# Performance work log

Measured on AMD Instinct MI355X. Metric: run time of the kernel, lower is better.

Reference implementation:

```python
import jax, jax.numpy as jnp
import numpy as np

N_NODES = 100000
N_EDGES = 1600000
IN_DIM = 256
OUT_DIM = 128
BATCH = 8192
SLOPE = 0.1
EPS = 1e-8


def setup_inputs() -> dict:
    key = jax.random.key(0)
    k1, k2, k3, k4, k5, k6, k7 = jax.random.split(key, 7)
    feats = jax.random.normal(k1, (N_NODES, IN_DIM), dtype=jnp.float32)
    W = jax.random.normal(k2, (IN_DIM, OUT_DIM), dtype=jnp.float32) / np.sqrt(IN_DIM)
    b = jax.random.normal(k3, (OUT_DIM,), dtype=jnp.float32) * 0.01
    a = jax.random.normal(k4, (2 * OUT_DIM,), dtype=jnp.float32) / np.sqrt(2 * OUT_DIM)
    r = jax.random.randint(k5, (N_EDGES,), 0, N_NODES, dtype=jnp.int64)
    c = jax.random.randint(k6, (N_EDGES,), 0, N_NODES, dtype=jnp.int64)
    batch_idx = jax.random.randint(k7, (BATCH,), 0, N_NODES, dtype=jnp.int64)
    return {"feats": feats, "W": W, "b": b, "a": a, "r": r, "c": c, "batch_idx": batch_idx}


def reference(feats, W, b, a, r, c, batch_idx):
    d = W.shape[1]
    new_emb = feats @ W + b                      # [N, d]
    # [h_r || h_c] @ a  ==  h_r @ a[:d] + h_c @ a[d:]
    s_src = new_emb @ a[:d]                      # [N]
    s_dst = new_emb @ a[d:]                      # [N]
    e = jnp.exp(jax.nn.leaky_relu(s_src[r] + s_dst[c], negative_slope=SLOPE))  # [E]
    denom = jax.ops.segment_sum(e, r, num_segments=N_NODES)                    # [N]
    num = jax.ops.segment_sum(e[:, None] * new_emb[c], r, num_segments=N_NODES)  # [N, d]
    out = num / (denom[:, None] + EPS)
    return out[batch_idx]
```

## Files before the change

kernel.cpp:

```cpp
#include <hip/hip_runtime.h>

#define N_NODES 100000
#define N_EDGES 1600000
#define IN_DIM  256
#define OUT_DIM 128
#define BATCH_N 8192
#define SLOPE   0.1f
#define EPS_V   1e-8f
#define BUCKET_CAP 96

__global__ __launch_bounds__(256) void setup_kernel(const float* __restrict__ W,
                                                    const float* __restrict__ b,
                                                    const float* __restrict__ a,
                                                    const int* __restrict__ batch_idx,
                                                    int* __restrict__ slot,
                                                    int* __restrict__ cursor,
                                                    float* __restrict__ uv,
                                                    float* __restrict__ consts) {
  const int blk = blockIdx.x, t = threadIdx.x;
  if (blk < 32) {
    int i = blk * 256 + t;
    slot[batch_idx[i]] = i;
    cursor[i] = 0;
    return;
  }
  float su = 0.f, sv = 0.f;
  for (int j = 0; j < OUT_DIM; j++) {
    float w = W[t * OUT_DIM + j];
    su += w * a[j];
    sv += w * a[OUT_DIM + j];
  }
  uv[t] = su;
  uv[IN_DIM + t] = sv;

  __shared__ float red[256];
  float pb = (t < OUT_DIM) ? b[t] : 0.f;
  red[t] = (t < OUT_DIM) ? pb * a[t] : 0.f;
  __syncthreads();
  for (int off = 128; off > 0; off >>= 1) {
    if (t < off) red[t] += red[t + off];
    __syncthreads();
  }
  if (t == 0) consts[0] = red[0];
  __syncthreads();
  red[t] = (t < OUT_DIM) ? pb * a[OUT_DIM + t] : 0.f;
  __syncthreads();
  for (int off = 128; off > 0; off >>= 1) {
    if (t < off) red[t] += red[t + off];
    __syncthreads();
  }
  if (t == 0) consts[1] = red[0];
}

__global__ __launch_bounds__(256) void scores_kernel(const float* __restrict__ feats,
                                                     const float* __restrict__ uv,
                                                     const float* __restrict__ consts,
                                                     float* __restrict__ s_src,
                                                     float* __restrict__ s_dst) {
  int wid = (blockIdx.x * blockDim.x + threadIdx.x) >> 6;
  int lane = threadIdx.x & 63;
  if (wid >= N_NODES) return;
  float4 f  = *(const float4*)&feats[(size_t)wid * IN_DIM + lane * 4];
  float4 u4 = *(const float4*)&uv[lane * 4];
  float4 v4 = *(const float4*)&uv[IN_DIM + lane * 4];
  float p1 = f.x * u4.x + f.y * u4.y + f.z * u4.z + f.w * u4.w;
  float p2 = f.x * v4.x + f.y * v4.y + f.z * v4.z + f.w * v4.w;
#pragma unroll
  for (int s = 32; s > 0; s >>= 1) {
    p1 += __shfl_xor(p1, s);
    p2 += __shfl_xor(p2, s);
  }
  if (lane == 0) {
    s_src[wid] = p1 + consts[0];
    s_dst[wid] = p2 + consts[1];
  }
}

__global__ __launch_bounds__(256) void scatter_kernel(const int* __restrict__ r, const int* __restrict__ c,
                                                      const int* __restrict__ slot,
                                                      const int* __restrict__ batch_idx,
                                                      const float* __restrict__ s_src,
                                                      const float* __restrict__ s_dst,
                                                      int* __restrict__ cursor,
                                                      int* __restrict__ bucket_c, float* __restrict__ bucket_e) {
  int i = blockIdx.x * blockDim.x + threadIdx.x;
  if (i >= N_EDGES) return;
  int rr = r[i];
  int sl = slot[rr];
  if (sl < 0 || sl >= BATCH_N) return;
  if (batch_idx[sl] != rr) return;
  int cc = c[i];
  float x = s_src[rr] + s_dst[cc];
  float lr = x > 0.f ? x : SLOPE * x;
  float e = expf(lr);
  int pos = atomicAdd(&cursor[sl], 1);
  if (pos < BUCKET_CAP) {
    bucket_c[sl * BUCKET_CAP + pos] = cc;
    bucket_e[sl * BUCKET_CAP + pos] = e;
  }
}

__global__ __launch_bounds__(256) void agg_kernel(const float* __restrict__ feats,
                                                  const int* __restrict__ cursor,
                                                  const int* __restrict__ bucket_c,
                                                  const float* __restrict__ bucket_e,
                                                  float* __restrict__ aggw,
                                                  float* __restrict__ scale_b) {
  __shared__ int   sc[BUCKET_CAP];
  __shared__ float se[BUCKET_CAP];
  __shared__ float red[4][256];
  __shared__ float dred[4];
  const int sl = blockIdx.x;
  const int t = threadIdx.x, w = t >> 6, lane = t & 63;
  int cnt = cursor[sl];
  cnt = cnt > BUCKET_CAP ? BUCKET_CAP : cnt;
  if (t < cnt) {
    sc[t] = bucket_c[sl * BUCKET_CAP + t];
    se[t] = bucket_e[sl * BUCKET_CAP + t];
  }
  __syncthreads();
  float ax = 0.f, ay = 0.f, az = 0.f, aw = 0.f, den = 0.f;
#pragma unroll 2
  for (int j = w; j < cnt; j += 4) {
    int cc  = sc[j];
    float e = se[j];
    float4 f = *(const float4*)&feats[(size_t)cc * IN_DIM + lane * 4];
    ax += e * f.x; ay += e * f.y; az += e * f.z; aw += e * f.w;
    den += e;
  }
  *(float4*)&red[w][lane * 4] = make_float4(ax, ay, az, aw);
  if (lane == 0) dred[w] = den;
  __syncthreads();
  if (w == 0) {
    float4 r0 = *(float4*)&red[0][lane * 4];
    float4 r1 = *(float4*)&red[1][lane * 4];
    float4 r2 = *(float4*)&red[2][lane * 4];
    float4 r3 = *(float4*)&red[3][lane * 4];
    float d = dred[0] + dred[1] + dred[2] + dred[3];
    float dinv = 1.f / (d + EPS_V);
    *(float4*)&aggw[(size_t)sl * IN_DIM + lane * 4] =
        make_float4((r0.x + r1.x + r2.x + r3.x) * dinv,
                    (r0.y + r1.y + r2.y + r3.y) * dinv,
                    (r0.z + r1.z + r2.z + r3.z) * dinv,
                    (r0.w + r1.w + r2.w + r3.w) * dinv);
    if (lane == 0) scale_b[sl] = d * dinv;
  }
}

__global__ __launch_bounds__(256) void gemm2_kernel(const float* __restrict__ aggw,
                                                    const float* __restrict__ W,
                                                    const float* __restrict__ b,
                                                    const float* __restrict__ scale_b,
                                                    const int* __restrict__ batch_idx,
                                                    const int* __restrict__ slot,
                                                    float* __restrict__ out) {
  __shared__ float As[32][33];
  __shared__ float Ws[32][128];
  __shared__ int ridx[32];
  const int t = threadIdx.x;
  const int row0 = blockIdx.x * 32;
  const int tx = t & 31;
  const int ty = t >> 5;

  if (t < 32) ridx[t] = slot[batch_idx[row0 + t]];
  __syncthreads();

  float acc[4][4];
#pragma unroll
  for (int i = 0; i < 4; i++)
#pragma unroll
    for (int j = 0; j < 4; j++) acc[i][j] = 0.f;

  for (int k0 = 0; k0 < IN_DIM; k0 += 32) {
    {
      int row = t >> 3, c4 = t & 7;
      float4 v = *(const float4*)&aggw[(size_t)ridx[row] * IN_DIM + k0 + c4 * 4];
      As[c4 * 4 + 0][row] = v.x;
      As[c4 * 4 + 1][row] = v.y;
      As[c4 * 4 + 2][row] = v.z;
      As[c4 * 4 + 3][row] = v.w;
    }
#pragma unroll
    for (int p = 0; p < 4; p++) {
      int id = t + p * 256;
      int kr = id >> 5, c4 = id & 31;
      *(float4*)&Ws[kr][c4 * 4] = *(const float4*)&W[(size_t)(k0 + kr) * OUT_DIM + c4 * 4];
    }
    __syncthreads();
#pragma unroll
    for (int k = 0; k < 32; k++) {
      float av[4];
#pragma unroll
      for (int i = 0; i < 4; i++) av[i] = As[k][ty * 4 + i];
      float4 w4 = *(const float4*)&Ws[k][tx * 4];
#pragma unroll
      for (int i = 0; i < 4; i++) {
        acc[i][0] += av[i] * w4.x; acc[i][1] += av[i] * w4.y;
        acc[i][2] += av[i] * w4.z; acc[i][3] += av[i] * w4.w;
      }
    }
    __syncthreads();
  }
  float4 b4 = *(const float4*)&b[tx * 4];
#pragma unroll
  for (int i = 0; i < 4; i++) {
    int row = row0 + ty * 4 + i;
    float sb = scale_b[ridx[ty * 4 + i]];
    *(float4*)&out[(size_t)row * OUT_DIM + tx * 4] =
        make_float4(acc[i][0] + sb * b4.x, acc[i][1] + sb * b4.y,
                    acc[i][2] + sb * b4.z, acc[i][3] + sb * b4.w);
  }
}

extern "C" void kernel_launch(void* const* d_in, const int* in_sizes, int n_in,
                              void* d_out, int out_size, void* d_ws, size_t ws_size,
                              hipStream_t stream) {
  const float* feats     = (const float*)d_in[0];
  const float* W         = (const float*)d_in[1];
  const float* b         = (const float*)d_in[2];
  const float* a         = (const float*)d_in[3];
  const int*   r         = (const int*)d_in[4];
  const int*   c         = (const int*)d_in[5];
  const int*   batch_idx = (const int*)d_in[6];
  float* out = (float*)d_out;

  float* uv       = (float*)d_ws;
  float* consts   = uv + 2 * IN_DIM;
  float* s_src    = consts + 8;
  float* s_dst    = s_src + N_NODES;
  int*   slot     = (int*)(s_dst + N_NODES);
  int*   cursor   = slot + N_NODES;
  float* scale_b  = (float*)(cursor + BATCH_N);
  int*   bucket_c = (int*)(scale_b + BATCH_N);
  float* bucket_e = (float*)(bucket_c + (size_t)BATCH_N * BUCKET_CAP);
  float* aggw     = bucket_e + (size_t)BATCH_N * BUCKET_CAP;

  setup_kernel<<<33, 256, 0, stream>>>(W, b, a, batch_idx, slot, cursor, uv, consts);
  scores_kernel<<<(N_NODES * 64 + 255) / 256, 256, 0, stream>>>(feats, uv, consts, s_src, s_dst);
  scatter_kernel<<<(N_EDGES + 255) / 256, 256, 0, stream>>>(r, c, slot, batch_idx, s_src, s_dst,
                                                            cursor, bucket_c, bucket_e);
  agg_kernel<<<BATCH_N, 256, 0, stream>>>(feats, cursor, bucket_c, bucket_e, aggw, scale_b);
  gemm2_kernel<<<BATCH_N / 32, 256, 0, stream>>>(aggw, W, b, scale_b, batch_idx, slot, out);
}
```

Before: 228.3 us.

## Compute attention scores lazily inside aggregation instead of for all nodes

Removes the scores kernel that computed s_src/s_dst for all 100k nodes, which read the full feature matrix. Source scores are now computed once per batch row and destination scores per edge inside the aggregation kernel, reusing the feature row it already loads. The scatter kernel no longer computes exp or writes edge weights. In exchange each edge adds a wave-wide shuffle reduction in the aggregation loop.

```diff
diff --git a/kernel.cpp b/kernel.cpp
--- a/kernel.cpp
+++ b/kernel.cpp
@@ -52,79 +52,60 @@
   if (t == 0) consts[1] = red[0];
 }
 
-__global__ __launch_bounds__(256) void scores_kernel(const float* __restrict__ feats,
-                                                     const float* __restrict__ uv,
-                                                     const float* __restrict__ consts,
-                                                     float* __restrict__ s_src,
-                                                     float* __restrict__ s_dst) {
-  int wid = (blockIdx.x * blockDim.x + threadIdx.x) >> 6;
-  int lane = threadIdx.x & 63;
-  if (wid >= N_NODES) return;
-  float4 f  = *(const float4*)&feats[(size_t)wid * IN_DIM + lane * 4];
-  float4 u4 = *(const float4*)&uv[lane * 4];
-  float4 v4 = *(const float4*)&uv[IN_DIM + lane * 4];
-  float p1 = f.x * u4.x + f.y * u4.y + f.z * u4.z + f.w * u4.w;
-  float p2 = f.x * v4.x + f.y * v4.y + f.z * v4.z + f.w * v4.w;
-#pragma unroll
-  for (int s = 32; s > 0; s >>= 1) {
-    p1 += __shfl_xor(p1, s);
-    p2 += __shfl_xor(p2, s);
-  }
-  if (lane == 0) {
-    s_src[wid] = p1 + consts[0];
-    s_dst[wid] = p2 + consts[1];
-  }
-}
-
 __global__ __launch_bounds__(256) void scatter_kernel(const int* __restrict__ r, const int* __restrict__ c,
                                                       const int* __restrict__ slot,
                                                       const int* __restrict__ batch_idx,
-                                                      const float* __restrict__ s_src,
-                                                      const float* __restrict__ s_dst,
                                                       int* __restrict__ cursor,
-                                                      int* __restrict__ bucket_c, float* __restrict__ bucket_e) {
+                                                      int* __restrict__ bucket_c) {
   int i = blockIdx.x * blockDim.x + threadIdx.x;
   if (i >= N_EDGES) return;
   int rr = r[i];
   int sl = slot[rr];
-  if (sl < 0 || sl >= BATCH_N) return;
+  if ((unsigned)sl >= (unsigned)BATCH_N) return;
   if (batch_idx[sl] != rr) return;
-  int cc = c[i];
-  float x = s_src[rr] + s_dst[cc];
-  float lr = x > 0.f ? x : SLOPE * x;
-  float e = expf(lr);
   int pos = atomicAdd(&cursor[sl], 1);
-  if (pos < BUCKET_CAP) {
-    bucket_c[sl * BUCKET_CAP + pos] = cc;
-    bucket_e[sl * BUCKET_CAP + pos] = e;
-  }
+  if (pos < BUCKET_CAP) bucket_c[sl * BUCKET_CAP + pos] = c[i];
 }
 
 __global__ __launch_bounds__(256) void agg_kernel(const float* __restrict__ feats,
                                                   const int* __restrict__ cursor,
                                                   const int* __restrict__ bucket_c,
-                                                  const float* __restrict__ bucket_e,
+                                                  const int* __restrict__ batch_idx,
+                                                  const float* __restrict__ uv,
+                                                  const float* __restrict__ consts,
                                                   float* __restrict__ aggw,
                                                   float* __restrict__ scale_b) {
   __shared__ int   sc[BUCKET_CAP];
-  __shared__ float se[BUCKET_CAP];
   __shared__ float red[4][256];
   __shared__ float dred[4];
   const int sl = blockIdx.x;
   const int t = threadIdx.x, w = t >> 6, lane = t & 63;
   int cnt = cursor[sl];
   cnt = cnt > BUCKET_CAP ? BUCKET_CAP : cnt;
-  if (t < cnt) {
-    sc[t] = bucket_c[sl * BUCKET_CAP + t];
-    se[t] = bucket_e[sl * BUCKET_CAP + t];
-  }
-  __syncthreads();
+  if (t < cnt) sc[t] = bucket_c[sl * BUCKET_CAP + t];
+
+  float4 u4 = *(const float4*)&uv[lane * 4];
+  float4 v4 = *(const float4*)&uv[IN_DIM + lane * 4];
+  int node = batch_idx[sl];
+  float4 fr = *(const float4*)&feats[(size_t)node * IN_DIM + lane * 4];
+  float p1 = fr.x * u4.x + fr.y * u4.y + fr.z * u4.z + fr.w * u4.w;
+#pragma unroll
+  for (int s2 = 32; s2 > 0; s2 >>= 1) p1 += __shfl_xor(p1, s2);
+  const float ssrc = p1 + consts[0];
+  const float cv = consts[1];
+  __syncthreads();
+
   float ax = 0.f, ay = 0.f, az = 0.f, aw = 0.f, den = 0.f;
 #pragma unroll 2
   for (int j = w; j < cnt; j += 4) {
-    int cc  = sc[j];
-    float e = se[j];
+    int cc = sc[j];
     float4 f = *(const float4*)&feats[(size_t)cc * IN_DIM + lane * 4];
+    float p2 = f.x * v4.x + f.y * v4.y + f.z * v4.z + f.w * v4.w;
+#pragma unroll
+    for (int s2 = 32; s2 > 0; s2 >>= 1) p2 += __shfl_xor(p2, s2);
+    float x = ssrc + p2 + cv;
+    float lr = x > 0.f ? x : SLOPE * x;
+    float e = expf(lr);
     ax += e * f.x; ay += e * f.y; az += e * f.z; aw += e * f.w;
     den += e;
   }
@@ -226,19 +207,16 @@
 
   float* uv       = (float*)d_ws;
   float* consts   = uv + 2 * IN_DIM;
-  float* s_src    = consts + 8;
-  float* s_dst    = s_src + N_NODES;
-  int*   slot     = (int*)(s_dst + N_NODES);
+  int*   slot     = (int*)(consts + 8);
   int*   cursor   = slot + N_NODES;
   float* scale_b  = (float*)(cursor + BATCH_N);
   int*   bucket_c = (int*)(scale_b + BATCH_N);
-  float* bucket_e = (float*)(bucket_c + (size_t)BATCH_N * BUCKET_CAP);
-  float* aggw     = bucket_e + (size_t)BATCH_N * BUCKET_CAP;
+  float* aggw     = (float*)(bucket_c + (size_t)BATCH_N * BUCKET_CAP);
 
   setup_kernel<<<33, 256, 0, stream>>>(W, b, a, batch_idx, slot, cursor, uv, consts);
-  scores_kernel<<<(N_NODES * 64 + 255) / 256, 256, 0, stream>>>(feats, uv, consts, s_src, s_dst);
-  scatter_kernel<<<(N_EDGES + 255) / 256, 256, 0, stream>>>(r, c, slot, batch_idx, s_src, s_dst,
-                                                            cursor, bucket_c, bucket_e);
-  agg_kernel<<<BATCH_N, 256, 0, stream>>>(feats, cursor, bucket_c, bucket_e, aggw, scale_b);
+  scatter_kernel<<<(N_EDGES + 255) / 256, 256, 0, stream>>>(r, c, slot, batch_idx,
+                                                            cursor, bucket_c);
+  agg_kernel<<<BATCH_N, 256, 0, stream>>>(feats, cursor, bucket_c, batch_idx, uv, consts,
+                                          aggw, scale_b);
   gemm2_kernel<<<BATCH_N / 32, 256, 0, stream>>>(aggw, W, b, scale_b, batch_idx, slot, out);
 }
```

Result: faster. 215.8 us (-5.5%).
